# Kernel tuning notes

Hardware: AMD Instinct MI355X
Metric: run time of the kernel (lower is better)

The kernel has to match this reference:

```python
import jax, jax.numpy as jnp
import numpy as np

B, N, K, PC, NC = 4, 4096, 20, 6, 13


def setup_inputs() -> dict:
    key = jax.random.key(0)
    ks = jax.random.split(key, 32)
    dims = [(12, 64), (64, 64), (128, 64), (64, 64), (128, 64), (192, 1024), (1216, 512), (512, 256)]
    inp = {"x": jax.random.normal(ks[0], (B, N, PC), jnp.float32)}
    for j, (ci, co) in enumerate(dims, 1):
        inp[f"w{j}"] = jax.random.normal(ks[j], (co, ci), jnp.float32) * (1.0 / np.sqrt(ci))
        # BatchNorm (eval mode) folded to per-channel affine: y = h*s + b
        inp[f"s{j}"] = jnp.ones((co,), jnp.float32) + 0.01 * jax.random.normal(ks[10 + j], (co,), jnp.float32)
        inp[f"b{j}"] = 0.01 * jax.random.normal(ks[20 + j], (co,), jnp.float32)
    inp["w9"] = jax.random.normal(ks[30], (NC, 256), jnp.float32) * (1.0 / np.sqrt(256))
    inp["b9"] = 0.01 * jax.random.normal(ks[31], (NC,), jnp.float32)
    return inp


def _lrelu(h):
    return jnp.where(h >= 0, h, 0.2 * h)


def _knn_idx(y, k):
    # y: (B, C, N); pairwise_distance = -||xi - xj||^2, topk -> nearest neighbors
    xx = jnp.sum(y * y, axis=1)                       # (B, N)
    inner = jnp.einsum('bcn,bcm->bnm', y, y)          # (B, N, N)
    pd = 2.0 * inner - xx[:, :, None] - xx[:, None, :]
    return jax.lax.top_k(pd, k)[1]                    # (B, N, k) int32


def _graph_feature(y, k):
    # y: (B, C, N) -> edge features (B, 2C, N, k): concat(neighbor - x, x)
    idx = _knn_idx(y, k)
    yt = jnp.transpose(y, (0, 2, 1))                  # (B, N, C)
    nb = jax.vmap(lambda f, i: f[i])(yt, idx)         # (B, N, k, C)
    c = yt[:, :, None, :]
    feat = jnp.concatenate([nb - c, jnp.broadcast_to(c, nb.shape)], axis=-1)
    return jnp.transpose(feat, (0, 3, 1, 2))          # (B, 2C, N, k)


def _conv2(f, w, s, b):
    # 1x1 Conv2d (no bias) + folded BN + LeakyReLU(0.2)
    h = jnp.einsum('oc,bcnk->bonk', w, f)
    return _lrelu(h * s[None, :, None, None] + b[None, :, None, None])


def _conv1(f, w, s, b):
    h = jnp.einsum('oc,bcn->bon', w, f)
    return _lrelu(h * s[None, :, None] + b[None, :, None])


def _forward(x, w1, s1, b1, w2, s2, b2, w3, s3, b3, w4, s4, b4, w5, s5, b5,
             w6, s6, b6, w7, s7, b7, w8, s8, b8, w9, b9):
    y = jnp.transpose(x, (0, 2, 1))                   # (B, C, N)
    f = _graph_feature(y, K)
    h = _conv2(f, w1, s1, b1)
    h = _conv2(h, w2, s2, b2)
    x1 = h.max(axis=-1)                               # (B, 64, N)
    f = _graph_feature(x1, K)
    h = _conv2(f, w3, s3, b3)
    h = _conv2(h, w4, s4, b4)
    x2 = h.max(axis=-1)
    f = _graph_feature(x2, K)
    h = _conv2(f, w5, s5, b5)
    x3 = h.max(axis=-1)
    cat = jnp.concatenate([x1, x2, x3], axis=1)       # (B, 192, N)
    g = _conv1(cat, w6, s6, b6).max(axis=-1, keepdims=True)  # (B, 1024, 1)
    g = jnp.broadcast_to(g, (g.shape[0], g.shape[1], x1.shape[-1]))
    h = jnp.concatenate([g, x1, x2, x3], axis=1)      # (B, 1216, N)
    h = _conv1(h, w7, s7, b7)
    h = _conv1(h, w8, s8, b8)
    # dropout is identity in eval mode
    out = jnp.einsum('oc,bcn->bon', w9, h) + b9[None, :, None]
    return out                                        # (B, NC, N)


def reference(x, w1, s1, b1, w2, s2, b2, w3, s3, b3, w4, s4, b4, w5, s5, b5,
              w6, s6, b6, w7, s7, b7, w8, s8, b8, w9, b9):
    return _forward(x, w1, s1, b1, w2, s2, b2, w3, s3, b3, w4, s4, b4, w5, s5, b5,
                    w6, s6, b6, w7, s7, b7, w8, s8, b8, w9, b9)
```

## Files before the change

kernel.cpp:

```cpp
#include <hip/hip_runtime.h>
#include <hip/hip_bf16.h>
#include <cstdint>
#include <cstddef>

#define NB 4
#define NPTS 4096
#define KK 20

typedef unsigned int u32;
typedef unsigned long long u64;

__device__ __forceinline__ float lrelu(float v) { return v >= 0.f ? v : 0.2f * v; }

__device__ __forceinline__ u32 fmap(float f) {
  u32 u = __float_as_uint(f);
  return (int)u < 0 ? ~u : (u | 0x80000000u);
}

__device__ __forceinline__ u64 wmax64(u64 v) {
#pragma unroll
  for (int o = 32; o >= 1; o >>= 1) {
    u64 t = __shfl_xor(v, o, 64);
    v = t > v ? t : v;
  }
  return v;
}

template <int C>
__global__ void k_sq(const float* __restrict__ f, float* __restrict__ xx) {
  int p = blockIdx.x * 256 + threadIdx.x;
  const float* fp = f + (size_t)p * C;
  float s = 0.f;
  if constexpr ((C & 3) == 0) {
#pragma unroll
    for (int c = 0; c < C; c += 4) {
      float4 v = *reinterpret_cast<const float4*>(fp + c);
      s += v.x * v.x + v.y * v.y + v.z * v.z + v.w * v.w;
    }
  } else {
#pragma unroll
    for (int c = 0; c < C; c++) s += fp[c] * fp[c];
  }
  xx[p] = s;
}

__global__ __launch_bounds__(512) void k_knn6(const float* __restrict__ f,
                                              const float* __restrict__ xx,
                                              int* __restrict__ idxo,
                                              int* __restrict__ flg) {
  __shared__ float chunkl[6 * 65];
  const int tid = threadIdx.x, wv = tid >> 6, lane = tid & 63;
  const int row = blockIdx.x * 8 + wv;
  const int b = row >> 12;
  const float xi = xx[row];

  float y[6];
#pragma unroll
  for (int c = 0; c < 6; c++) y[c] = f[(size_t)row * 6 + c];

  u64 t0 = 0, t1 = 0, t2 = 0, t3 = 0;

  for (int jc = 0; jc < NPTS / 64; jc++) {
    __syncthreads();
    for (int t = tid; t < 64 * 6; t += 512) {
      int j = t / 6, c = t - j * 6;
      chunkl[c * 65 + j] = f[(size_t)(b * NPTS + jc * 64 + j) * 6 + c];
    }
    __syncthreads();
    const float xj = xx[b * NPTS + jc * 64 + lane];
    float acc = 0.f;
#pragma unroll
    for (int c = 0; c < 6; c++) acc = fmaf(chunkl[c * 65 + lane], y[c], acc);
    const float s = fmaf(2.f, acc, -xi) - xj;
    const u64 key = ((u64)fmap(s) << 32) | (u64)(~(u32)(jc * 64 + lane));
    if (key > t3) {
      u64 a0 = t0, a1 = t1, a2 = t2;
      bool g0 = key > a0, g1 = key > a1, g2 = key > a2;
      t0 = g0 ? key : a0;
      t1 = g0 ? a0 : (g1 ? key : a1);
      t2 = g1 ? a1 : (g2 ? key : a2);
      t3 = g2 ? a2 : key;
    }
  }

  u64 h = t0, n1 = t1, n2 = t2, n3 = t3;
  int pops = 0, myj = 0;
  for (int m = 0; m < KK; m++) {
    u64 wm = wmax64(h);
    int j = (int)(~(u32)wm) & (NPTS - 1);
    if (lane == m) myj = j;
    if (h == wm) { h = n1; n1 = n2; n2 = n3; n3 = 0; pops++; }
  }
  u64 bad = __ballot(pops >= 4);
  if (lane < KK) idxo[(size_t)row * KK + lane] = myj;
  if (lane == 0) flg[row] = (bad != 0ull) ? 1 : 0;
}

__global__ __launch_bounds__(512, 2) void k_knn64(const float* __restrict__ f,
                                                  const float* __restrict__ xx,
                                                  int* __restrict__ idxo,
                                                  int* __restrict__ flg) {
  __shared__ float ch[4][64 * 68];
  const int tid = threadIdx.x, wv = tid >> 6, lane = tid & 63;
  const int rowbase = blockIdx.x * 32;
  const int b = rowbase >> 12;
  const float* fb = f + (size_t)b * NPTS * 64;
  const int r0 = rowbase + wv * 4;
  const float* yrow = f + (size_t)r0 * 64;

  float xi[4];
#pragma unroll
  for (int r = 0; r < 4; r++) xi[r] = xx[r0 + r];

  u64 t0[4], t1[4], t2[4], t3[4];
#pragma unroll
  for (int r = 0; r < 4; r++) { t0[r] = 0; t1[r] = 0; t2[r] = 0; t3[r] = 0; }

#pragma unroll 1
  for (int jp = 0; jp < NPTS / 256; jp++) {
#pragma unroll 1
    for (int k = 0; k < 8; k++) {
      int flat = k * 512 + tid;
      int row = flat >> 4, q = flat & 15;
      float4 v = *reinterpret_cast<const float4*>(
          fb + (size_t)(jp * 256 + row) * 64 + 4 * q);
      *reinterpret_cast<float4*>(&ch[row >> 6][(row & 63) * 68 + 4 * q]) = v;
    }
    __syncthreads();

    float acc[4][4];
#pragma unroll
    for (int r = 0; r < 4; r++)
#pragma unroll
      for (int u = 0; u < 4; u++) acc[r][u] = 0.f;
#pragma unroll 1
    for (int q = 0; q < 16; q++) {
      const float4 c0 = *reinterpret_cast<const float4*>(&ch[0][lane * 68 + 4 * q]);
      const float4 c1 = *reinterpret_cast<const float4*>(&ch[1][lane * 68 + 4 * q]);
      const float4 c2 = *reinterpret_cast<const float4*>(&ch[2][lane * 68 + 4 * q]);
      const float4 c3 = *reinterpret_cast<const float4*>(&ch[3][lane * 68 + 4 * q]);
#pragma unroll
      for (int r = 0; r < 4; r++) {
        const float4 yq = *reinterpret_cast<const float4*>(yrow + r * 64 + 4 * q);
        acc[r][0] = fmaf(c0.x, yq.x, acc[r][0]);
        acc[r][0] = fmaf(c0.y, yq.y, acc[r][0]);
        acc[r][0] = fmaf(c0.z, yq.z, acc[r][0]);
        acc[r][0] = fmaf(c0.w, yq.w, acc[r][0]);
        acc[r][1] = fmaf(c1.x, yq.x, acc[r][1]);
        acc[r][1] = fmaf(c1.y, yq.y, acc[r][1]);
        acc[r][1] = fmaf(c1.z, yq.z, acc[r][1]);
        acc[r][1] = fmaf(c1.w, yq.w, acc[r][1]);
        acc[r][2] = fmaf(c2.x, yq.x, acc[r][2]);
        acc[r][2] = fmaf(c2.y, yq.y, acc[r][2]);
        acc[r][2] = fmaf(c2.z, yq.z, acc[r][2]);
        acc[r][2] = fmaf(c2.w, yq.w, acc[r][2]);
        acc[r][3] = fmaf(c3.x, yq.x, acc[r][3]);
        acc[r][3] = fmaf(c3.y, yq.y, acc[r][3]);
        acc[r][3] = fmaf(c3.z, yq.z, acc[r][3]);
        acc[r][3] = fmaf(c3.w, yq.w, acc[r][3]);
      }
    }
    float xj[4];
    u32 jv[4];
#pragma unroll
    for (int u = 0; u < 4; u++) {
      xj[u] = xx[b * NPTS + jp * 256 + u * 64 + lane];
      jv[u] = ~(u32)(jp * 256 + u * 64 + lane);
    }
#pragma unroll
    for (int r = 0; r < 4; r++) {
#pragma unroll
      for (int u = 0; u < 4; u++) {
        const float s = fmaf(2.f, acc[r][u], -xi[r]) - xj[u];
        const u64 key = ((u64)fmap(s) << 32) | (u64)jv[u];
        if (key > t3[r]) {
          u64 a0 = t0[r], a1 = t1[r], a2 = t2[r];
          bool g0 = key > a0, g1 = key > a1, g2 = key > a2;
          t0[r] = g0 ? key : a0;
          t1[r] = g0 ? a0 : (g1 ? key : a1);
          t2[r] = g1 ? a1 : (g2 ? key : a2);
          t3[r] = g2 ? a2 : key;
        }
      }
    }
    __syncthreads();
  }

#pragma unroll
  for (int r = 0; r < 4; r++) {
    u64 h = t0[r], n1 = t1[r], n2 = t2[r], n3 = t3[r];
    int pops = 0, myj = 0;
    for (int m = 0; m < KK; m++) {
      u64 wm = wmax64(h);
      int j = (int)(~(u32)wm) & (NPTS - 1);
      if (lane == m) myj = j;
      if (h == wm) { h = n1; n1 = n2; n2 = n3; n3 = 0; pops++; }
    }
    u64 bad = __ballot(pops >= 4);
    if (lane < KK) idxo[(size_t)(r0 + r) * KK + lane] = myj;
    if (lane == 0) flg[r0 + r] = (bad != 0ull) ? 1 : 0;
  }
}

template <int C>
__global__ __launch_bounds__(64) void k_knn_fix(const float* __restrict__ f,
                                                const float* __restrict__ xx,
                                                int* __restrict__ idxo,
                                                const int* __restrict__ flg) {
  __shared__ u64 kl[NPTS];
  const int lane = threadIdx.x;
  for (int row = blockIdx.x; row < NB * NPTS; row += gridDim.x) {
    if (!flg[row]) continue;
    const int b = row >> 12;
    float yreg[C];
#pragma unroll
    for (int c = 0; c < C; c++) yreg[c] = f[(size_t)row * C + c];
    const float xi = xx[row];
    for (int jj = 0; jj < 64; jj++) {
      int j = jj * 64 + lane;
      const float* fp = f + (size_t)(b * NPTS + j) * C;
      float d = 0.f;
#pragma unroll
      for (int c = 0; c < C; c++) d = fmaf(yreg[c], fp[c], d);
      float s = fmaf(2.f, d, -xi) - xx[b * NPTS + j];
      kl[j] = ((u64)fmap(s) << 32) | (u64)(u32)(~(u32)j);
    }
    __syncthreads();
    int myj = 0;
    for (int m = 0; m < KK; m++) {
      u64 lm = 0;
      for (int jj = 0; jj < 64; jj++) {
        u64 v = kl[jj * 64 + lane];
        lm = v > lm ? v : lm;
      }
      u64 wm = wmax64(lm);
      int j = (int)(~(u32)wm) & (NPTS - 1);
      if (lane == m) myj = j;
      if (lane == (j & 63)) kl[j] = 0;
      __syncthreads();
    }
    if (lane < KK) idxo[row * KK + lane] = myj;
    __syncthreads();
  }
}

__global__ __launch_bounds__(256) void k_ec1(
    const float* __restrict__ x, const int* __restrict__ idx,
    const float* __restrict__ w1, const float* __restrict__ s1, const float* __restrict__ b1,
    const float* __restrict__ w2, const float* __restrict__ s2, const float* __restrict__ b2,
    float* __restrict__ out) {
  __shared__ float h1l[4][64];
  const int wv = threadIdx.x >> 6, lane = threadIdx.x & 63;
  float w1r[12];
#pragma unroll
  for (int c = 0; c < 12; c += 4) {
    float4 v = *reinterpret_cast<const float4*>(w1 + lane * 12 + c);
    w1r[c] = v.x; w1r[c + 1] = v.y; w1r[c + 2] = v.z; w1r[c + 3] = v.w;
  }
  float w2r[64];
#pragma unroll
  for (int c = 0; c < 64; c += 4) {
    float4 v = *reinterpret_cast<const float4*>(w2 + lane * 64 + c);
    w2r[c] = v.x; w2r[c + 1] = v.y; w2r[c + 2] = v.z; w2r[c + 3] = v.w;
  }
  const float sc1 = s1[lane], bc1 = b1[lane], sc2 = s2[lane], bc2 = b2[lane];
  const int wid = blockIdx.x * 4 + wv;
  for (int p = wid; p < NB * NPTS; p += 2048) {
    const float* cp = x + (size_t)p * 6;
    float c0 = cp[0], c1 = cp[1], c2 = cp[2], c3 = cp[3], c4 = cp[4], c5 = cp[5];
    const int bb = p >> 12;
    float m = -3.402823466e38f;
    for (int k = 0; k < KK; k++) {
      int nb = idx[p * KK + k];
      const float* nf = x + (size_t)((bb << 12) + nb) * 6;
      float e0 = nf[0] - c0, e1 = nf[1] - c1, e2 = nf[2] - c2;
      float e3 = nf[3] - c3, e4 = nf[4] - c4, e5 = nf[5] - c5;
      float h = w1r[0] * e0 + w1r[1] * e1 + w1r[2] * e2 + w1r[3] * e3 + w1r[4] * e4 +
                w1r[5] * e5 + w1r[6] * c0 + w1r[7] * c1 + w1r[8] * c2 + w1r[9] * c3 +
                w1r[10] * c4 + w1r[11] * c5;
      h = lrelu(fmaf(h, sc1, bc1));
      h1l[wv][lane] = h;
      float a0 = 0.f, a1 = 0.f;
#pragma unroll
      for (int c = 0; c < 64; c += 8) {
        float4 hv = *reinterpret_cast<const float4*>(&h1l[wv][c]);
        float4 hw = *reinterpret_cast<const float4*>(&h1l[wv][c + 4]);
        a0 = fmaf(w2r[c], hv.x, a0); a0 = fmaf(w2r[c + 1], hv.y, a0);
        a0 = fmaf(w2r[c + 2], hv.z, a0); a0 = fmaf(w2r[c + 3], hv.w, a0);
        a1 = fmaf(w2r[c + 4], hw.x, a1); a1 = fmaf(w2r[c + 5], hw.y, a1);
        a1 = fmaf(w2r[c + 6], hw.z, a1); a1 = fmaf(w2r[c + 7], hw.w, a1);
      }
      m = fmaxf(m, lrelu(fmaf(a0 + a1, sc2, bc2)));
    }
    out[(size_t)p * 64 + lane] = m;
  }
}

template <bool HAS2>
__global__ __launch_bounds__(256, 1) void k_ec2(
    const float* __restrict__ xin, const int* __restrict__ idx,
    const float* __restrict__ w3, const float* __restrict__ s3, const float* __restrict__ b3,
    const float* __restrict__ w4, const float* __restrict__ s4, const float* __restrict__ b4,
    float* __restrict__ out) {
  __shared__ float ctl[4][64];
  __shared__ float nbl[4][64];
  __shared__ float h1l[4][64];
  const int wv = threadIdx.x >> 6, lane = threadIdx.x & 63;
  float wa[64], wb[64];
#pragma unroll
  for (int c = 0; c < 64; c += 4) {
    float4 va = *reinterpret_cast<const float4*>(w3 + (size_t)lane * 128 + c);
    float4 vb = *reinterpret_cast<const float4*>(w3 + (size_t)lane * 128 + 64 + c);
    wa[c] = va.x; wa[c + 1] = va.y; wa[c + 2] = va.z; wa[c + 3] = va.w;
    wb[c] = vb.x - va.x; wb[c + 1] = vb.y - va.y; wb[c + 2] = vb.z - va.z; wb[c + 3] = vb.w - va.w;
  }
  float w4r[64];
  if constexpr (HAS2) {
#pragma unroll
    for (int c = 0; c < 64; c += 4) {
      float4 v = *reinterpret_cast<const float4*>(w4 + (size_t)lane * 64 + c);
      w4r[c] = v.x; w4r[c + 1] = v.y; w4r[c + 2] = v.z; w4r[c + 3] = v.w;
    }
  }
  const float sc3 = s3[lane], bc3 = b3[lane];
  float sc4 = 0.f, bc4 = 0.f;
  if constexpr (HAS2) { sc4 = s4[lane]; bc4 = b4[lane]; }
  const int wid = blockIdx.x * 4 + wv;
  for (int p = wid; p < NB * NPTS; p += 2048) {
    const int bb = p >> 12;
    ctl[wv][lane] = xin[(size_t)p * 64 + lane];
    float d0 = 0.f, d1 = 0.f;
#pragma unroll
    for (int c = 0; c < 64; c += 8) {
      float4 cv = *reinterpret_cast<const float4*>(&ctl[wv][c]);
      float4 cw = *reinterpret_cast<const float4*>(&ctl[wv][c + 4]);
      d0 = fmaf(wb[c], cv.x, d0); d0 = fmaf(wb[c + 1], cv.y, d0);
      d0 = fmaf(wb[c + 2], cv.z, d0); d0 = fmaf(wb[c + 3], cv.w, d0);
      d1 = fmaf(wb[c + 4], cw.x, d1); d1 = fmaf(wb[c + 5], cw.y, d1);
      d1 = fmaf(wb[c + 6], cw.z, d1); d1 = fmaf(wb[c + 7], cw.w, d1);
    }
    const float cd = d0 + d1;
    float m = -3.402823466e38f;
    for (int k = 0; k < KK; k++) {
      int nb = idx[p * KK + k];
      nbl[wv][lane] = xin[(size_t)((bb << 12) + nb) * 64 + lane];
      float a0 = cd, a1 = 0.f;
#pragma unroll
      for (int c = 0; c < 64; c += 8) {
        float4 nv = *reinterpret_cast<const float4*>(&nbl[wv][c]);
        float4 nw = *reinterpret_cast<const float4*>(&nbl[wv][c + 4]);
        a0 = fmaf(wa[c], nv.x, a0); a0 = fmaf(wa[c + 1], nv.y, a0);
        a0 = fmaf(wa[c + 2], nv.z, a0); a0 = fmaf(wa[c + 3], nv.w, a0);
        a1 = fmaf(wa[c + 4], nw.x, a1); a1 = fmaf(wa[c + 5], nw.y, a1);
        a1 = fmaf(wa[c + 6], nw.z, a1); a1 = fmaf(wa[c + 7], nw.w, a1);
      }
      float h = lrelu(fmaf(a0 + a1, sc3, bc3));
      if constexpr (HAS2) {
        h1l[wv][lane] = h;
        float q0 = 0.f, q1 = 0.f;
#pragma unroll
        for (int c = 0; c < 64; c += 8) {
          float4 hv = *reinterpret_cast<const float4*>(&h1l[wv][c]);
          float4 hw = *reinterpret_cast<const float4*>(&h1l[wv][c + 4]);
          q0 = fmaf(w4r[c], hv.x, q0); q0 = fmaf(w4r[c + 1], hv.y, q0);
          q0 = fmaf(w4r[c + 2], hv.z, q0); q0 = fmaf(w4r[c + 3], hv.w, q0);
          q1 = fmaf(w4r[c + 4], hw.x, q1); q1 = fmaf(w4r[c + 5], hw.y, q1);
          q1 = fmaf(w4r[c + 6], hw.z, q1); q1 = fmaf(w4r[c + 7], hw.w, q1);
        }
        m = fmaxf(m, lrelu(fmaf(q0 + q1, sc4, bc4)));
      } else {
        m = fmaxf(m, h);
      }
    }
    out[(size_t)p * 64 + lane] = m;
  }
}

__global__ __launch_bounds__(256) void k_conv6(
    const float* __restrict__ x1, const float* __restrict__ x2, const float* __restrict__ x3,
    const float* __restrict__ w6, const float* __restrict__ s6, const float* __restrict__ b6,
    float* __restrict__ gpart) {
  __shared__ float Wl[64 * 68];
  __shared__ float Xl[64 * 68];
  __shared__ float mxl[16][64];
  const int tid = threadIdx.x;
  const int cot = blockIdx.x & 15;
  const int ptb = blockIdx.x >> 4;
  const int co0 = (tid & 15) * 4;
  const int n0 = (tid >> 4) * 4;
  const int sr = tid >> 2;
  const int sci = (tid & 3) * 16;
  float scv[4], bcv[4];
#pragma unroll
  for (int i = 0; i < 4; i++) {
    scv[i] = s6[cot * 64 + co0 + i];
    bcv[i] = b6[cot * 64 + co0 + i];
  }
  float mx[4];
#pragma unroll
  for (int i = 0; i < 4; i++) mx[i] = -3.402823466e38f;

  for (int half = 0; half < 2; half++) {
    float acc[4][4];
#pragma unroll
    for (int i = 0; i < 4; i++)
#pragma unroll
      for (int j = 0; j < 4; j++) acc[i][j] = 0.f;
    for (int cib = 0; cib < 3; cib++) {
      const float* xsel = cib == 0 ? x1 : cib == 1 ? x2 : x3;
      __syncthreads();
      {
        const float* ws_ = w6 + (size_t)(cot * 64 + sr) * 192 + cib * 64 + sci;
#pragma unroll
        for (int s = 0; s < 16; s += 4) {
          float4 v = *reinterpret_cast<const float4*>(ws_ + s);
          Wl[(sci + s) * 68 + sr] = v.x;
          Wl[(sci + s + 1) * 68 + sr] = v.y;
          Wl[(sci + s + 2) * 68 + sr] = v.z;
          Wl[(sci + s + 3) * 68 + sr] = v.w;
        }
        const float* xs = xsel + (size_t)(ptb * 128 + half * 64 + sr) * 64 + sci;
#pragma unroll
        for (int s = 0; s < 16; s += 4) {
          float4 v = *reinterpret_cast<const float4*>(xs + s);
          Xl[(sci + s) * 68 + sr] = v.x;
          Xl[(sci + s + 1) * 68 + sr] = v.y;
          Xl[(sci + s + 2) * 68 + sr] = v.z;
          Xl[(sci + s + 3) * 68 + sr] = v.w;
        }
      }
      __syncthreads();
#pragma unroll 8
      for (int ci = 0; ci < 64; ci++) {
        float4 wv = *reinterpret_cast<const float4*>(&Wl[ci * 68 + co0]);
        float4 xv = *reinterpret_cast<const float4*>(&Xl[ci * 68 + n0]);
        acc[0][0] = fmaf(wv.x, xv.x, acc[0][0]);
        acc[0][1] = fmaf(wv.x, xv.y, acc[0][1]);
        acc[0][2] = fmaf(wv.x, xv.z, acc[0][2]);
        acc[0][3] = fmaf(wv.x, xv.w, acc[0][3]);
        acc[1][0] = fmaf(wv.y, xv.x, acc[1][0]);
        acc[1][1] = fmaf(wv.y, xv.y, acc[1][1]);
        acc[1][2] = fmaf(wv.y, xv.z, acc[1][2]);
        acc[1][3] = fmaf(wv.y, xv.w, acc[1][3]);
        acc[2][0] = fmaf(wv.z, xv.x, acc[2][0]);
        acc[2][1] = fmaf(wv.z, xv.y, acc[2][1]);
        acc[2][2] = fmaf(wv.z, xv.z, acc[2][2]);
        acc[2][3] = fmaf(wv.z, xv.w, acc[2][3]);
        acc[3][0] = fmaf(wv.w, xv.x, acc[3][0]);
        acc[3][1] = fmaf(wv.w, xv.y, acc[3][1]);
        acc[3][2] = fmaf(wv.w, xv.z, acc[3][2]);
        acc[3][3] = fmaf(wv.w, xv.w, acc[3][3]);
      }
    }
#pragma unroll
    for (int i = 0; i < 4; i++)
#pragma unroll
      for (int j = 0; j < 4; j++)
        mx[i] = fmaxf(mx[i], lrelu(fmaf(acc[i][j], scv[i], bcv[i])));
  }
  __syncthreads();
#pragma unroll
  for (int i = 0; i < 4; i++) mxl[tid >> 4][co0 + i] = mx[i];
  __syncthreads();
  if (tid < 64) {
    float m = -3.402823466e38f;
#pragma unroll
    for (int g = 0; g < 16; g++) m = fmaxf(m, mxl[g][tid]);
    const int b = ptb >> 5, ch = ptb & 31;
    gpart[(size_t)(b * 32 + ch) * 1024 + cot * 64 + tid] = m;
  }
}

__global__ void k_gred(const float* __restrict__ gpart, float* __restrict__ g) {
  int t = blockIdx.x * 256 + threadIdx.x;
  int b = t >> 10, co = t & 1023;
  float m = -3.402823466e38f;
  for (int ch = 0; ch < 32; ch++) m = fmaxf(m, gpart[(size_t)(b * 32 + ch) * 1024 + co]);
  g[t] = m;
}

__global__ void k_gc(const float* __restrict__ w7, const float* __restrict__ g,
                     float* __restrict__ gcv) {
  int t = blockIdx.x * 256 + threadIdx.x;
  int b = t >> 9, co = t & 511;
  const float* gr = g + b * 1024;
  const float* wr = w7 + (size_t)co * 1216;
  float a0 = 0.f, a1 = 0.f, a2 = 0.f, a3 = 0.f;
  for (int ci = 0; ci < 1024; ci += 4) {
    float4 wv = *reinterpret_cast<const float4*>(wr + ci);
    float4 gv = *reinterpret_cast<const float4*>(gr + ci);
    a0 = fmaf(wv.x, gv.x, a0); a1 = fmaf(wv.y, gv.y, a1);
    a2 = fmaf(wv.z, gv.z, a2); a3 = fmaf(wv.w, gv.w, a3);
  }
  gcv[t] = (a0 + a1) + (a2 + a3);
}

__global__ __launch_bounds__(256) void k_conv7(
    const float* __restrict__ x1, const float* __restrict__ x2, const float* __restrict__ x3,
    const float* __restrict__ gcv, const float* __restrict__ w7,
    const float* __restrict__ s7, const float* __restrict__ b7,
    float* __restrict__ h7, int bbase) {
  __shared__ float Wl[64 * 68];
  __shared__ float Xl[64 * 68];
  const int tid = threadIdx.x;
  const int cot = blockIdx.x & 7;
  const int nt = blockIdx.x >> 3;
  const int co0 = (tid & 15) * 4;
  const int n0 = (tid >> 4) * 4;
  const int sr = tid >> 2;
  const int sci = (tid & 3) * 16;
  float acc[4][4];
#pragma unroll
  for (int i = 0; i < 4; i++)
#pragma unroll
    for (int j = 0; j < 4; j++) acc[i][j] = 0.f;

  for (int cib = 0; cib < 3; cib++) {
    const float* xsel = cib == 0 ? x1 : cib == 1 ? x2 : x3;
    __syncthreads();
    {
      const float* ws_ = w7 + (size_t)(cot * 64 + sr) * 1216 + 1024 + cib * 64 + sci;
#pragma unroll
      for (int s = 0; s < 16; s += 4) {
        float4 v = *reinterpret_cast<const float4*>(ws_ + s);
        Wl[(sci + s) * 68 + sr] = v.x;
        Wl[(sci + s + 1) * 68 + sr] = v.y;
        Wl[(sci + s + 2) * 68 + sr] = v.z;
        Wl[(sci + s + 3) * 68 + sr] = v.w;
      }
      const float* xs = xsel + (size_t)(bbase * NPTS + nt * 64 + sr) * 64 + sci;
#pragma unroll
      for (int s = 0; s < 16; s += 4) {
        float4 v = *reinterpret_cast<const float4*>(xs + s);
        Xl[(sci + s) * 68 + sr] = v.x;
        Xl[(sci + s + 1) * 68 + sr] = v.y;
        Xl[(sci + s + 2) * 68 + sr] = v.z;
        Xl[(sci + s + 3) * 68 + sr] = v.w;
      }
    }
    __syncthreads();
#pragma unroll 8
    for (int ci = 0; ci < 64; ci++) {
      float4 wv = *reinterpret_cast<const float4*>(&Wl[ci * 68 + co0]);
      float4 xv = *reinterpret_cast<const float4*>(&Xl[ci * 68 + n0]);
      acc[0][0] = fmaf(wv.x, xv.x, acc[0][0]);
      acc[0][1] = fmaf(wv.x, xv.y, acc[0][1]);
      acc[0][2] = fmaf(wv.x, xv.z, acc[0][2]);
      acc[0][3] = fmaf(wv.x, xv.w, acc[0][3]);
      acc[1][0] = fmaf(wv.y, xv.x, acc[1][0]);
      acc[1][1] = fmaf(wv.y, xv.y, acc[1][1]);
      acc[1][2] = fmaf(wv.y, xv.z, acc[1][2]);
      acc[1][3] = fmaf(wv.y, xv.w, acc[1][3]);
      acc[2][0] = fmaf(wv.z, xv.x, acc[2][0]);
      acc[2][1] = fmaf(wv.z, xv.y, acc[2][1]);
      acc[2][2] = fmaf(wv.z, xv.z, acc[2][2]);
      acc[2][3] = fmaf(wv.z, xv.w, acc[2][3]);
      acc[3][0] = fmaf(wv.w, xv.x, acc[3][0]);
      acc[3][1] = fmaf(wv.w, xv.y, acc[3][1]);
      acc[3][2] = fmaf(wv.w, xv.z, acc[3][2]);
      acc[3][3] = fmaf(wv.w, xv.w, acc[3][3]);
    }
  }
  const int b = bbase + (nt >> 6);
  float scv[4], bcv[4], g0v[4];
#pragma unroll
  for (int i = 0; i < 4; i++) {
    scv[i] = s7[cot * 64 + co0 + i];
    bcv[i] = b7[cot * 64 + co0 + i];
    g0v[i] = gcv[b * 512 + cot * 64 + co0 + i];
  }
#pragma unroll
  for (int j = 0; j < 4; j++) {
    float4 o;
    o.x = lrelu(fmaf(acc[0][j] + g0v[0], scv[0], bcv[0]));
    o.y = lrelu(fmaf(acc[1][j] + g0v[1], scv[1], bcv[1]));
    o.z = lrelu(fmaf(acc[2][j] + g0v[2], scv[2], bcv[2]));
    o.w = lrelu(fmaf(acc[3][j] + g0v[3], scv[3], bcv[3]));
    *reinterpret_cast<float4*>(
        &h7[(size_t)(nt * 64 + n0 + j) * 512 + cot * 64 + co0]) = o;
  }
}

__global__ __launch_bounds__(256) void k_conv8(
    const float* __restrict__ h7, const float* __restrict__ w8,
    const float* __restrict__ s8, const float* __restrict__ b8,
    float* __restrict__ h8, int bbase) {
  __shared__ float Wl[64 * 68];
  __shared__ float Xl[64 * 68];
  const int tid = threadIdx.x;
  const int cot = blockIdx.x & 3;
  const int nt = blockIdx.x >> 2;
  const int co0 = (tid & 15) * 4;
  const int n0 = (tid >> 4) * 4;
  const int sr = tid >> 2;
  const int sci = (tid & 3) * 16;
  float acc[4][4];
#pragma unroll
  for (int i = 0; i < 4; i++)
#pragma unroll
    for (int j = 0; j < 4; j++) acc[i][j] = 0.f;

  for (int cib = 0; cib < 512; cib += 64) {
    __syncthreads();
    {
      const float* ws_ = w8 + (size_t)(cot * 64 + sr) * 512 + cib + sci;
#pragma unroll
      for (int s = 0; s < 16; s += 4) {
        float4 v = *reinterpret_cast<const float4*>(ws_ + s);
        Wl[(sci + s) * 68 + sr] = v.x;
        Wl[(sci + s + 1) * 68 + sr] = v.y;
        Wl[(sci + s + 2) * 68 + sr] = v.z;
        Wl[(sci + s + 3) * 68 + sr] = v.w;
      }
      const float* xs = h7 + (size_t)(nt * 64 + sr) * 512 + cib + sci;
#pragma unroll
      for (int s = 0; s < 16; s += 4) {
        float4 v = *reinterpret_cast<const float4*>(xs + s);
        Xl[(sci + s) * 68 + sr] = v.x;
        Xl[(sci + s + 1) * 68 + sr] = v.y;
        Xl[(sci + s + 2) * 68 + sr] = v.z;
        Xl[(sci + s + 3) * 68 + sr] = v.w;
      }
    }
    __syncthreads();
#pragma unroll 8
    for (int ci = 0; ci < 64; ci++) {
      float4 wv = *reinterpret_cast<const float4*>(&Wl[ci * 68 + co0]);
      float4 xv = *reinterpret_cast<const float4*>(&Xl[ci * 68 + n0]);
      acc[0][0] = fmaf(wv.x, xv.x, acc[0][0]);
      acc[0][1] = fmaf(wv.x, xv.y, acc[0][1]);
      acc[0][2] = fmaf(wv.x, xv.z, acc[0][2]);
      acc[0][3] = fmaf(wv.x, xv.w, acc[0][3]);
      acc[1][0] = fmaf(wv.y, xv.x, acc[1][0]);
      acc[1][1] = fmaf(wv.y, xv.y, acc[1][1]);
      acc[1][2] = fmaf(wv.y, xv.z, acc[1][2]);
      acc[1][3] = fmaf(wv.y, xv.w, acc[1][3]);
      acc[2][0] = fmaf(wv.z, xv.x, acc[2][0]);
      acc[2][1] = fmaf(wv.z, xv.y, acc[2][1]);
      acc[2][2] = fmaf(wv.z, xv.z, acc[2][2]);
      acc[2][3] = fmaf(wv.z, xv.w, acc[2][3]);
      acc[3][0] = fmaf(wv.w, xv.x, acc[3][0]);
      acc[3][1] = fmaf(wv.w, xv.y, acc[3][1]);
      acc[3][2] = fmaf(wv.w, xv.z, acc[3][2]);
      acc[3][3] = fmaf(wv.w, xv.w, acc[3][3]);
    }
  }
  float scv[4], bcv[4];
#pragma unroll
  for (int i = 0; i < 4; i++) {
    scv[i] = s8[cot * 64 + co0 + i];
    bcv[i] = b8[cot * 64 + co0 + i];
  }
#pragma unroll
  for (int j = 0; j < 4; j++) {
    float4 o;
    o.x = lrelu(fmaf(acc[0][j], scv[0], bcv[0]));
    o.y = lrelu(fmaf(acc[1][j], scv[1], bcv[1]));
    o.z = lrelu(fmaf(acc[2][j], scv[2], bcv[2]));
    o.w = lrelu(fmaf(acc[3][j], scv[3], bcv[3]));
    *reinterpret_cast<float4*>(
        &h8[(size_t)(bbase * NPTS + nt * 64 + n0 + j) * 256 + cot * 64 + co0]) = o;
  }
}

__global__ __launch_bounds__(256) void k_conv9(const float* __restrict__ h8,
                                               const float* __restrict__ w9,
                                               const float* __restrict__ b9,
                                               float* __restrict__ outp) {
  __shared__ float Wl[16 * 256];
  __shared__ float Xl[64 * 68];
  const int tid = threadIdx.x;
  for (int q = tid; q < 16 * 256; q += 256) Wl[q] = q < 13 * 256 ? w9[q] : 0.f;
  const int p = tid & 63, cg = tid >> 6;
  const int sr = tid >> 2, sci = (tid & 3) * 16;
  float acc[4] = {0.f, 0.f, 0.f, 0.f};
  for (int cib = 0; cib < 256; cib += 64) {
    __syncthreads();
    {
      const float* xs = h8 + (size_t)(blockIdx.x * 64 + sr) * 256 + cib + sci;
#pragma unroll
      for (int s = 0; s < 16; s += 4) {
        float4 v = *reinterpret_cast<const float4*>(xs + s);
        Xl[(sci + s) * 68 + sr] = v.x;
        Xl[(sci + s + 1) * 68 + sr] = v.y;
        Xl[(sci + s + 2) * 68 + sr] = v.z;
        Xl[(sci + s + 3) * 68 + sr] = v.w;
      }
    }
    __syncthreads();
#pragma unroll 8
    for (int ci = 0; ci < 64; ci++) {
      float xv = Xl[ci * 68 + p];
#pragma unroll
      for (int q = 0; q < 4; q++)
        acc[q] = fmaf(Wl[(cg * 4 + q) * 256 + cib + ci], xv, acc[q]);
    }
  }
  const int pg = blockIdx.x * 64 + p;
  const int bb = pg >> 12, n = pg & (NPTS - 1);
#pragma unroll
  for (int q = 0; q < 4; q++) {
    int co = cg * 4 + q;
    if (co < 13) outp[(size_t)(bb * 13 + co) * NPTS + n] = acc[q] + b9[co];
  }
}

extern "C" void kernel_launch(void* const* d_in, const int* in_sizes, int n_in,
                              void* d_out, int out_size, void* d_ws, size_t ws_size,
                              hipStream_t stream) {
  const float* x = (const float*)d_in[0];
  const float* w1 = (const float*)d_in[1];
  const float* s1 = (const float*)d_in[2];
  const float* b1 = (const float*)d_in[3];
  const float* w2 = (const float*)d_in[4];
  const float* s2 = (const float*)d_in[5];
  const float* b2 = (const float*)d_in[6];
  const float* w3 = (const float*)d_in[7];
  const float* s3 = (const float*)d_in[8];
  const float* b3 = (const float*)d_in[9];
  const float* w4 = (const float*)d_in[10];
  const float* s4 = (const float*)d_in[11];
  const float* b4 = (const float*)d_in[12];
  const float* w5 = (const float*)d_in[13];
  const float* s5 = (const float*)d_in[14];
  const float* b5 = (const float*)d_in[15];
  const float* w6 = (const float*)d_in[16];
  const float* s6 = (const float*)d_in[17];
  const float* b6 = (const float*)d_in[18];
  const float* w7 = (const float*)d_in[19];
  const float* s7 = (const float*)d_in[20];
  const float* b7 = (const float*)d_in[21];
  const float* w8 = (const float*)d_in[22];
  const float* s8 = (const float*)d_in[23];
  const float* b8 = (const float*)d_in[24];
  const float* w9 = (const float*)d_in[25];
  const float* b9 = (const float*)d_in[26];

  float* ws = (float*)d_ws;
  float* xxp = ws + 0;
  int* idxp = (int*)(ws + 16384);
  int* flg = (int*)(ws + 344064);
  float* x1 = ws + 360448;
  float* x2 = ws + 1409024;
  float* x3 = ws + 2457600;
  float* gpart = ws + 3506176;
  float* g = ws + 3637248;
  float* gcv = ws + 3641344;
  float* h7 = ws + 3643392;
  float* h8 = ws + 7837696;

  k_sq<6><<<64, 256, 0, stream>>>(x, xxp);
  k_knn6<<<2048, 512, 0, stream>>>(x, xxp, idxp, flg);
  k_knn_fix<6><<<512, 64, 0, stream>>>(x, xxp, idxp, flg);
  k_ec1<<<512, 256, 0, stream>>>(x, idxp, w1, s1, b1, w2, s2, b2, x1);
  k_sq<64><<<64, 256, 0, stream>>>(x1, xxp);
  k_knn64<<<512, 512, 0, stream>>>(x1, xxp, idxp, flg);
  k_knn_fix<64><<<512, 64, 0, stream>>>(x1, xxp, idxp, flg);
  k_ec2<true><<<512, 256, 0, stream>>>(x1, idxp, w3, s3, b3, w4, s4, b4, x2);
  k_sq<64><<<64, 256, 0, stream>>>(x2, xxp);
  k_knn64<<<512, 512, 0, stream>>>(x2, xxp, idxp, flg);
  k_knn_fix<64><<<512, 64, 0, stream>>>(x2, xxp, idxp, flg);
  k_ec2<false><<<512, 256, 0, stream>>>(x2, idxp, w5, s5, b5, nullptr, nullptr, nullptr, x3);
  k_conv6<<<2048, 256, 0, stream>>>(x1, x2, x3, w6, s6, b6, gpart);
  k_gred<<<16, 256, 0, stream>>>(gpart, g);
  k_gc<<<8, 256, 0, stream>>>(w7, g, gcv);
  for (int bbase = 0; bbase < NB; bbase += 2) {
    k_conv7<<<1024, 256, 0, stream>>>(x1, x2, x3, gcv, w7, s7, b7, h7, bbase);
    k_conv8<<<512, 256, 0, stream>>>(h7, w8, s8, b8, h8, bbase);
  }
  k_conv9<<<256, 256, 0, stream>>>(h8, w9, b9, (float*)d_out);
}
```

Measured before the change: 1.864 ms.

## Prefetch next neighbor in edge-conv loops, widen accumulators, split k_gc reduction

In the edge-conv kernels, the next neighbor's features are now loaded before the current neighbor's dot products run, so gather latency is hidden behind compute. The 64-wide dot products now use four independent accumulators instead of two to shorten FMA dependency chains. k_gc now splits each output's 1024-long dot product across 8 threads and combines them through shared memory, so it launches 64 blocks instead of 8 and fills more of the GPU. The kNN inner loop is also unrolled by 2, which may add register pressure.

```diff
diff --git a/kernel.cpp b/kernel.cpp
--- a/kernel.cpp
+++ b/kernel.cpp
@@ -133,7 +133,7 @@
     for (int r = 0; r < 4; r++)
 #pragma unroll
       for (int u = 0; u < 4; u++) acc[r][u] = 0.f;
-#pragma unroll 1
+#pragma unroll 2
     for (int q = 0; q < 16; q++) {
       const float4 c0 = *reinterpret_cast<const float4*>(&ch[0][lane * 68 + 4 * q]);
       const float4 c1 = *reinterpret_cast<const float4*>(&ch[1][lane * 68 + 4 * q]);
@@ -270,27 +270,44 @@
     float c0 = cp[0], c1 = cp[1], c2 = cp[2], c3 = cp[3], c4 = cp[4], c5 = cp[5];
     const int bb = p >> 12;
     float m = -3.402823466e38f;
+    int nb = idx[p * KK];
+    float n0v[6];
+    {
+      const float* nf = x + (size_t)((bb << 12) + nb) * 6;
+#pragma unroll
+      for (int c = 0; c < 6; c++) n0v[c] = nf[c];
+    }
     for (int k = 0; k < KK; k++) {
-      int nb = idx[p * KK + k];
-      const float* nf = x + (size_t)((bb << 12) + nb) * 6;
-      float e0 = nf[0] - c0, e1 = nf[1] - c1, e2 = nf[2] - c2;
-      float e3 = nf[3] - c3, e4 = nf[4] - c4, e5 = nf[5] - c5;
+      float e0 = n0v[0] - c0, e1 = n0v[1] - c1, e2 = n0v[2] - c2;
+      float e3 = n0v[3] - c3, e4 = n0v[4] - c4, e5 = n0v[5] - c5;
+      if (k + 1 < KK) {
+        int nb2 = idx[p * KK + k + 1];
+        const float* nf = x + (size_t)((bb << 12) + nb2) * 6;
+#pragma unroll
+        for (int c = 0; c < 6; c++) n0v[c] = nf[c];
+      }
       float h = w1r[0] * e0 + w1r[1] * e1 + w1r[2] * e2 + w1r[3] * e3 + w1r[4] * e4 +
                 w1r[5] * e5 + w1r[6] * c0 + w1r[7] * c1 + w1r[8] * c2 + w1r[9] * c3 +
                 w1r[10] * c4 + w1r[11] * c5;
       h = lrelu(fmaf(h, sc1, bc1));
       h1l[wv][lane] = h;
-      float a0 = 0.f, a1 = 0.f;
-#pragma unroll
-      for (int c = 0; c < 64; c += 8) {
-        float4 hv = *reinterpret_cast<const float4*>(&h1l[wv][c]);
-        float4 hw = *reinterpret_cast<const float4*>(&h1l[wv][c + 4]);
-        a0 = fmaf(w2r[c], hv.x, a0); a0 = fmaf(w2r[c + 1], hv.y, a0);
-        a0 = fmaf(w2r[c + 2], hv.z, a0); a0 = fmaf(w2r[c + 3], hv.w, a0);
-        a1 = fmaf(w2r[c + 4], hw.x, a1); a1 = fmaf(w2r[c + 5], hw.y, a1);
-        a1 = fmaf(w2r[c + 6], hw.z, a1); a1 = fmaf(w2r[c + 7], hw.w, a1);
-      }
-      m = fmaxf(m, lrelu(fmaf(a0 + a1, sc2, bc2)));
+      float a0 = 0.f, a1 = 0.f, a2 = 0.f, a3 = 0.f;
+#pragma unroll
+      for (int c = 0; c < 64; c += 16) {
+        float4 h0 = *reinterpret_cast<const float4*>(&h1l[wv][c]);
+        float4 h1 = *reinterpret_cast<const float4*>(&h1l[wv][c + 4]);
+        float4 h2 = *reinterpret_cast<const float4*>(&h1l[wv][c + 8]);
+        float4 h3 = *reinterpret_cast<const float4*>(&h1l[wv][c + 12]);
+        a0 = fmaf(w2r[c], h0.x, a0); a0 = fmaf(w2r[c + 1], h0.y, a0);
+        a0 = fmaf(w2r[c + 2], h0.z, a0); a0 = fmaf(w2r[c + 3], h0.w, a0);
+        a1 = fmaf(w2r[c + 4], h1.x, a1); a1 = fmaf(w2r[c + 5], h1.y, a1);
+        a1 = fmaf(w2r[c + 6], h1.z, a1); a1 = fmaf(w2r[c + 7], h1.w, a1);
+        a2 = fmaf(w2r[c + 8], h2.x, a2); a2 = fmaf(w2r[c + 9], h2.y, a2);
+        a2 = fmaf(w2r[c + 10], h2.z, a2); a2 = fmaf(w2r[c + 11], h2.w, a2);
+        a3 = fmaf(w2r[c + 12], h3.x, a3); a3 = fmaf(w2r[c + 13], h3.y, a3);
+        a3 = fmaf(w2r[c + 14], h3.z, a3); a3 = fmaf(w2r[c + 15], h3.w, a3);
+      }
+      m = fmaxf(m, lrelu(fmaf((a0 + a1) + (a2 + a3), sc2, bc2)));
     }
     out[(size_t)p * 64 + lane] = m;
   }
@@ -341,33 +358,47 @@
     }
     const float cd = d0 + d1;
     float m = -3.402823466e38f;
+    float cur = xin[(size_t)((bb << 12) + idx[p * KK]) * 64 + lane];
     for (int k = 0; k < KK; k++) {
-      int nb = idx[p * KK + k];
-      nbl[wv][lane] = xin[(size_t)((bb << 12) + nb) * 64 + lane];
-      float a0 = cd, a1 = 0.f;
-#pragma unroll
-      for (int c = 0; c < 64; c += 8) {
-        float4 nv = *reinterpret_cast<const float4*>(&nbl[wv][c]);
-        float4 nw = *reinterpret_cast<const float4*>(&nbl[wv][c + 4]);
-        a0 = fmaf(wa[c], nv.x, a0); a0 = fmaf(wa[c + 1], nv.y, a0);
-        a0 = fmaf(wa[c + 2], nv.z, a0); a0 = fmaf(wa[c + 3], nv.w, a0);
-        a1 = fmaf(wa[c + 4], nw.x, a1); a1 = fmaf(wa[c + 5], nw.y, a1);
-        a1 = fmaf(wa[c + 6], nw.z, a1); a1 = fmaf(wa[c + 7], nw.w, a1);
-      }
-      float h = lrelu(fmaf(a0 + a1, sc3, bc3));
+      nbl[wv][lane] = cur;
+      if (k + 1 < KK)
+        cur = xin[(size_t)((bb << 12) + idx[p * KK + k + 1]) * 64 + lane];
+      float a0 = cd, a1 = 0.f, a2 = 0.f, a3 = 0.f;
+#pragma unroll
+      for (int c = 0; c < 64; c += 16) {
+        float4 n0 = *reinterpret_cast<const float4*>(&nbl[wv][c]);
+        float4 n1 = *reinterpret_cast<const float4*>(&nbl[wv][c + 4]);
+        float4 n2 = *reinterpret_cast<const float4*>(&nbl[wv][c + 8]);
+        float4 n3 = *reinterpret_cast<const float4*>(&nbl[wv][c + 12]);
+        a0 = fmaf(wa[c], n0.x, a0); a0 = fmaf(wa[c + 1], n0.y, a0);
+        a0 = fmaf(wa[c + 2], n0.z, a0); a0 = fmaf(wa[c + 3], n0.w, a0);
+        a1 = fmaf(wa[c + 4], n1.x, a1); a1 = fmaf(wa[c + 5], n1.y, a1);
+        a1 = fmaf(wa[c + 6], n1.z, a1); a1 = fmaf(wa[c + 7], n1.w, a1);
+        a2 = fmaf(wa[c + 8], n2.x, a2); a2 = fmaf(wa[c + 9], n2.y, a2);
+        a2 = fmaf(wa[c + 10], n2.z, a2); a2 = fmaf(wa[c + 11], n2.w, a2);
+        a3 = fmaf(wa[c + 12], n3.x, a3); a3 = fmaf(wa[c + 13], n3.y, a3);
+        a3 = fmaf(wa[c + 14], n3.z, a3); a3 = fmaf(wa[c + 15], n3.w, a3);
+      }
+      float h = lrelu(fmaf((a0 + a1) + (a2 + a3), sc3, bc3));
       if constexpr (HAS2) {
         h1l[wv][lane] = h;
-        float q0 = 0.f, q1 = 0.f;
-#pragma unroll
-        for (int c = 0; c < 64; c += 8) {
-          float4 hv = *reinterpret_cast<const float4*>(&h1l[wv][c]);
-          float4 hw = *reinterpret_cast<const float4*>(&h1l[wv][c + 4]);
-          q0 = fmaf(w4r[c], hv.x, q0); q0 = fmaf(w4r[c + 1], hv.y, q0);
-          q0 = fmaf(w4r[c + 2], hv.z, q0); q0 = fmaf(w4r[c + 3], hv.w, q0);
-          q1 = fmaf(w4r[c + 4], hw.x, q1); q1 = fmaf(w4r[c + 5], hw.y, q1);
-          q1 = fmaf(w4r[c + 6], hw.z, q1); q1 = fmaf(w4r[c + 7], hw.w, q1);
+        float q0 = 0.f, q1 = 0.f, q2 = 0.f, q3 = 0.f;
+#pragma unroll
+        for (int c = 0; c < 64; c += 16) {
+          float4 h0 = *reinterpret_cast<const float4*>(&h1l[wv][c]);
+          float4 h1 = *reinterpret_cast<const float4*>(&h1l[wv][c + 4]);
+          float4 h2 = *reinterpret_cast<const float4*>(&h1l[wv][c + 8]);
+          float4 h3 = *reinterpret_cast<const float4*>(&h1l[wv][c + 12]);
+          q0 = fmaf(w4r[c], h0.x, q0); q0 = fmaf(w4r[c + 1], h0.y, q0);
+          q0 = fmaf(w4r[c + 2], h0.z, q0); q0 = fmaf(w4r[c + 3], h0.w, q0);
+          q1 = fmaf(w4r[c + 4], h1.x, q1); q1 = fmaf(w4r[c + 5], h1.y, q1);
+          q1 = fmaf(w4r[c + 6], h1.z, q1); q1 = fmaf(w4r[c + 7], h1.w, q1);
+          q2 = fmaf(w4r[c + 8], h2.x, q2); q2 = fmaf(w4r[c + 9], h2.y, q2);
+          q2 = fmaf(w4r[c + 10], h2.z, q2); q2 = fmaf(w4r[c + 11], h2.w, q2);
+          q3 = fmaf(w4r[c + 12], h3.x, q3); q3 = fmaf(w4r[c + 13], h3.y, q3);
+          q3 = fmaf(w4r[c + 14], h3.z, q3); q3 = fmaf(w4r[c + 15], h3.w, q3);
         }
-        m = fmaxf(m, lrelu(fmaf(q0 + q1, sc4, bc4)));
+        m = fmaxf(m, lrelu(fmaf((q0 + q1) + (q2 + q3), sc4, bc4)));
       } else {
         m = fmaxf(m, h);
       }
@@ -479,20 +510,33 @@
   g[t] = m;
 }
 
-__global__ void k_gc(const float* __restrict__ w7, const float* __restrict__ g,
-                     float* __restrict__ gcv) {
-  int t = blockIdx.x * 256 + threadIdx.x;
-  int b = t >> 9, co = t & 511;
-  const float* gr = g + b * 1024;
-  const float* wr = w7 + (size_t)co * 1216;
+__global__ __launch_bounds__(256) void k_gc(const float* __restrict__ w7,
+                                            const float* __restrict__ g,
+                                            float* __restrict__ gcv) {
+  __shared__ float red[256];
+  const int tid = threadIdx.x;
+  const int ol = tid >> 3;
+  const int seg = tid & 7;
+  const int t = blockIdx.x * 32 + ol;
+  const int b = t >> 9, co = t & 511;
+  const float* gr = g + b * 1024 + seg * 128;
+  const float* wr = w7 + (size_t)co * 1216 + seg * 128;
   float a0 = 0.f, a1 = 0.f, a2 = 0.f, a3 = 0.f;
-  for (int ci = 0; ci < 1024; ci += 4) {
+#pragma unroll 8
+  for (int ci = 0; ci < 128; ci += 4) {
     float4 wv = *reinterpret_cast<const float4*>(wr + ci);
     float4 gv = *reinterpret_cast<const float4*>(gr + ci);
     a0 = fmaf(wv.x, gv.x, a0); a1 = fmaf(wv.y, gv.y, a1);
     a2 = fmaf(wv.z, gv.z, a2); a3 = fmaf(wv.w, gv.w, a3);
   }
-  gcv[t] = (a0 + a1) + (a2 + a3);
+  red[tid] = (a0 + a1) + (a2 + a3);
+  __syncthreads();
+  if (seg == 0) {
+    float s = red[tid];
+#pragma unroll
+    for (int q = 1; q < 8; q++) s += red[tid + q];
+    gcv[t] = s;
+  }
 }
 
 __global__ __launch_bounds__(256) void k_conv7(
@@ -763,7 +807,7 @@
   k_ec2<false><<<512, 256, 0, stream>>>(x2, idxp, w5, s5, b5, nullptr, nullptr, nullptr, x3);
   k_conv6<<<2048, 256, 0, stream>>>(x1, x2, x3, w6, s6, b6, gpart);
   k_gred<<<16, 256, 0, stream>>>(gpart, g);
-  k_gc<<<8, 256, 0, stream>>>(w7, g, gcv);
+  k_gc<<<64, 256, 0, stream>>>(w7, g, gcv);
   for (int bbase = 0; bbase < NB; bbase += 2) {
     k_conv7<<<1024, 256, 0, stream>>>(x1, x2, x3, gcv, w7, s7, b7, h7, bbase);
     k_conv8<<<512, 256, 0, stream>>>(h7, w8, s8, b8, h8, bbase);
```

Measured after the change: 1.786 ms (median of 2 runs). 4.2% less time.
